# Kernel tuning notes

Hardware: AMD Instinct MI355X
Metric: run time of the kernel (lower is better)

Reference implementation:

```python
import jax, jax.numpy as jnp
import numpy as np
from jax import lax

C = 64
KD = 16  # in_channels // k_factor
KS = 3
DN = ('NCHW', 'OIHW', 'NCHW')


def setup_inputs() -> dict:
    key = jax.random.key(0)
    ks = jax.random.split(key, 9)
    B, H, W = 4, 128, 128
    s = 0.05
    return {
        'x': jax.random.normal(ks[0], (B, C, H, W), jnp.float32),
        'y': jax.random.normal(ks[1], (B, C, H, W), jnp.float32),
        'z': jax.random.normal(ks[2], (B, C, H, W), jnp.float32),
        'Wq': jax.random.normal(ks[3], (C, 1, KS, KS), jnp.float32) * s,   # depthwise
        'bq': jax.random.normal(ks[4], (C,), jnp.float32) * s,
        'Wk': jax.random.normal(ks[5], (KD, C, KS, KS), jnp.float32) * s,
        'bk': jax.random.normal(ks[6], (KD,), jnp.float32) * s,
        'wv': jax.random.normal(ks[7], (KD,), jnp.float32) * s,           # 1x1 conv 1->KD
        'bv': jax.random.normal(ks[8], (KD,), jnp.float32) * s,
    }


def reference(x, y, z, Wq, bq, Wk, bk, wv, bv):
    # Q: depthwise 3x3 conv + ReLU on y -> [B,C,H,W]
    q = jax.nn.relu(
        lax.conv_general_dilated(y, Wq, (1, 1), 'SAME',
                                 dimension_numbers=DN, feature_group_count=C)
        + bq[None, :, None, None])
    # K: 3x3 conv C->KD + ReLU on x -> [B,KD,H,W], shared across the C channel axis
    k = jax.nn.relu(
        lax.conv_general_dilated(x, Wk, (1, 1), 'SAME', dimension_numbers=DN)
        + bk[None, :, None, None])
    # V: 1x1 conv 1->KD + ReLU applied per input channel of z -> [B,C,KD,H,W]
    v = jax.nn.relu(z[:, :, None] * wv[None, None, :, None, None]
                    + bv[None, None, :, None, None])
    # Degenerate SDPA: head_dim=1 so scale=1; softmax over the KD 'sequence' axis.
    scores = q[:, :, None] * k[:, None]              # [B,C,KD,H,W]
    attn = jax.nn.softmax(scores, axis=2)
    return jnp.sum(attn * v, axis=2)                 # [B,C,H,W]
```

## Files before the change

### kernel.cpp

```cpp
#include <hip/hip_runtime.h>

#define HH 128
#define WW 128
#define CC 64
#define KD 16
#define HW (HH * WW)
#define HWB (HW * 4)
#define TOTBYTES (4u * CC * HW * 4u)
#define OOB_SENT 0x40000000

typedef __attribute__((ext_vector_type(4))) int   int32x4_t;
typedef __attribute__((ext_vector_type(4))) float floatx4;
typedef __attribute__((ext_vector_type(2))) float floatx2;

__device__ floatx4 llvm_amdgcn_raw_buffer_load_v4f32(int32x4_t srsrc, int voffset,
                                                     int soffset, int aux)
    __asm("llvm.amdgcn.raw.buffer.load.v4f32");
__device__ float llvm_amdgcn_raw_buffer_load_f32(int32x4_t srsrc, int voffset,
                                                 int soffset, int aux)
    __asm("llvm.amdgcn.raw.buffer.load.f32");

__device__ inline int32x4_t make_srd(const void* p, unsigned bytes) {
    const unsigned long long a = (unsigned long long)p;
    int32x4_t r;
    r.x = (int)(a & 0xffffffffull);
    r.y = (int)(a >> 32);
    r.z = (int)bytes;
    r.w = 0x00020000;
    return r;
}

#if __has_builtin(__builtin_amdgcn_exp2f)
#define FAST_EXP2(x) __builtin_amdgcn_exp2f(x)
#define KLOG2E 1.44269504088896340736f
#else
#define FAST_EXP2(x) __expf(x)
#define KLOG2E 1.0f
#endif

__global__ __launch_bounds__(512, 8) void gatev_fused(
    const float* __restrict__ x, const float* __restrict__ y,
    const float* __restrict__ z,
    const float* __restrict__ Wq, const float* __restrict__ bq,
    const float* __restrict__ Wk, const float* __restrict__ bk,
    const float* __restrict__ wv, const float* __restrict__ bv,
    float* __restrict__ out)
{
    __shared__ float wk_lds[9216];

    const int tid  = threadIdx.x;
    const int g    = __builtin_amdgcn_readfirstlane(tid >> 6);
    const int lane = tid & 63;
    const int px   = lane & 15, py = lane >> 4;
    const int b    = blockIdx.z;
    const int h    = blockIdx.y * 4 + py;
    const int w    = blockIdx.x * 16 + px;
    const int pix  = h * WW + w;

    const bool interior = (blockIdx.x > 0) & (blockIdx.x < 7) &
                          (blockIdx.y > 0) & (blockIdx.y < 31);

    const int32x4_t rx = make_srd(x, TOTBYTES);
    const int32x4_t ry = make_srd(y, TOTBYTES);
    const int32x4_t rz = make_srd(z, TOTBYTES);

    const int colb = (w > 0 ? w - 1 : 0) * 4;
    int rowB[3];
#pragma unroll
    for (int r = 0; r < 3; ++r) {
        const int rr = h - 1 + r;
        rowB[r] = (rr >= 0 && rr < HH) ? rr * WW * 4 + colb : OOB_SENT;
    }
    const float mL = (w > 0) ? 1.f : 0.f;
    const float mR = (w < WW - 1) ? 1.f : 0.f;
    const bool  w0e = (w == 0);

    const int base = b * CC * HWB;
    const int c0   = __builtin_amdgcn_readfirstlane(g * 8);

    {
        const int d  = tid & 15;
        const int cA = tid >> 4;
#pragma unroll
        for (int half = 0; half < 2; ++half) {
            const int c   = cA + half * 32;
            const int dst = (c >> 3) * 1152 + (c & 7) * 144 + d;
            const float* src = Wk + (d * CC + c) * 9;
#pragma unroll
            for (int t = 0; t < 9; ++t)
                wk_lds[dst + t * 16] = src[t];
        }
    }
    __syncthreads();

    floatx2 acc2[8];
#pragma unroll
    for (int p = 0; p < 8; ++p) acc2[p] = (floatx2){0.f, 0.f};

    auto load3 = [&](floatx4 (&f)[3], int so) {
#pragma unroll
        for (int r = 0; r < 3; ++r)
            f[r] = llvm_amdgcn_raw_buffer_load_v4f32(rx, rowB[r], so, 0);
    };
    auto taps3 = [&](const floatx4& f, float& tL, float& tC, float& tR) {
        if (interior) { tL = f.x; tC = f.y; tR = f.z; }
        else {
            tL = f.x * mL;
            tC = w0e ? f.x : f.y;
            tR = (w0e ? f.y : f.z) * mR;
        }
    };
    auto compute = [&](const floatx4 (&f)[3], int wb) {
        float tp[9];
#pragma unroll
        for (int r = 0; r < 3; ++r)
            taps3(f[r], tp[r * 3 + 0], tp[r * 3 + 1], tp[r * 3 + 2]);
#pragma unroll
        for (int t = 0; t < 9; ++t) {
            const floatx2 tp2 = {tp[t], tp[t]};
#pragma unroll
            for (int j = 0; j < 4; ++j) {
                const floatx4 w4 = *(const floatx4*)&wk_lds[wb + t * 16 + j * 4];
                const floatx2 lo = __builtin_shufflevector(w4, w4, 0, 1);
                const floatx2 hi = __builtin_shufflevector(w4, w4, 2, 3);
                acc2[2 * j + 0] = __builtin_elementwise_fma(lo, tp2, acc2[2 * j + 0]);
                acc2[2 * j + 1] = __builtin_elementwise_fma(hi, tp2, acc2[2 * j + 1]);
            }
        }
    };

    const int wbase = g * 1152;
    floatx4 f0[3], f1[3];
    load3(f0, base + c0 * HWB);
#pragma unroll
    for (int cp = 0; cp < 4; ++cp) {
        load3(f1, base + (c0 + 2 * cp + 1) * HWB);
        compute(f0, wbase + (2 * cp) * 144);
        load3(f0, base + (c0 + 2 * cp + 2) * HWB);
        compute(f1, wbase + (2 * cp + 1) * 144);
    }
    __syncthreads();

#pragma unroll
    for (int p = 0; p < 8; ++p) {
        wk_lds[g * 1024 + (2 * p + 0) * 64 + lane] = acc2[p].x;
        wk_lds[g * 1024 + (2 * p + 1) * 64 + lane] = acc2[p].y;
    }
    __syncthreads();

#pragma unroll
    for (int rep = 0; rep < 2; ++rep) {
        const int idx = tid + rep * 512;
        float s = wk_lds[idx];
#pragma unroll
        for (int gg = 1; gg < 8; ++gg) s += wk_lds[gg * 1024 + idx];
        const int d = idx >> 6;
        wk_lds[idx] = fmaxf(s + bk[d], 0.f) * KLOG2E;
    }
    __syncthreads();

    floatx2 qp[4], zp[4];
#pragma unroll 2
    for (int ci = 0; ci < 8; ++ci) {
        const int c  = c0 + ci;
        const int so = base + c * HWB;
        const float* wq = Wq + c * 9;
        float a = 0.f;
#pragma unroll
        for (int r = 0; r < 3; ++r) {
            const floatx4 f = llvm_amdgcn_raw_buffer_load_v4f32(ry, rowB[r], so, 0);
            float tL, tC, tR;
            taps3(f, tL, tC, tR);
            a = fmaf(wq[r * 3 + 0], tL, a);
            a = fmaf(wq[r * 3 + 1], tC, a);
            a = fmaf(wq[r * 3 + 2], tR, a);
        }
        qp[ci >> 1][ci & 1] = fmaxf(a + bq[c], 0.f);
        zp[ci >> 1][ci & 1] = llvm_amdgcn_raw_buffer_load_f32(rz, pix * 4, so, 0);
    }

    floatx2 num2[4], den2[4];
    const floatx2 zero2 = {0.f, 0.f};
#pragma unroll
    for (int p = 0; p < 4; ++p) { num2[p] = zero2; den2[p] = zero2; }

#pragma unroll
    for (int d = 0; d < KD; ++d) {
        const float kl  = wk_lds[d * 64 + lane];
        const floatx2 kl2 = {kl, kl};
        const float wvd = wv[d], bvd = bv[d];
        const floatx2 wv2 = {wvd, wvd}, bv2 = {bvd, bvd};
#pragma unroll
        for (int p = 0; p < 4; ++p) {
            const floatx2 s2 = qp[p] * kl2;
            floatx2 e2;
            e2.x = FAST_EXP2(s2.x);
            e2.y = FAST_EXP2(s2.y);
            const floatx2 v2 = __builtin_elementwise_max(
                __builtin_elementwise_fma(zp[p], wv2, bv2), zero2);
            num2[p] = __builtin_elementwise_fma(e2, v2, num2[p]);
            den2[p] = den2[p] + e2;
        }
    }

    float* ob = out + (size_t)b * CC * HW;
#pragma unroll
    for (int ci = 0; ci < 8; ++ci)
        ob[(c0 + ci) * HW + pix] =
            __fdividef(num2[ci >> 1][ci & 1], den2[ci >> 1][ci & 1]);
}

extern "C" void kernel_launch(void* const* d_in, const int* in_sizes, int n_in,
                              void* d_out, int out_size, void* d_ws, size_t ws_size,
                              hipStream_t stream) {
    const float* x  = (const float*)d_in[0];
    const float* y  = (const float*)d_in[1];
    const float* z  = (const float*)d_in[2];
    const float* Wq = (const float*)d_in[3];
    const float* bq = (const float*)d_in[4];
    const float* Wk = (const float*)d_in[5];
    const float* bk = (const float*)d_in[6];
    const float* wv = (const float*)d_in[7];
    const float* bv = (const float*)d_in[8];
    float* out = (float*)d_out;

    dim3 grid(WW / 16, HH / 4, 4);
    dim3 block(512);
    hipLaunchKernelGGL(gatev_fused, grid, block, 0, stream,
                       x, y, z, Wq, bq, Wk, bk, wv, bv, out);
}
```

Measured before the change: 50.49 us.

## Compute two adjacent pixels per thread to reuse conv taps and weights

Each thread now handles two horizontally adjacent pixels. A single float4 row load supplies the taps for both, and each LDS weight read feeds twice as many FMAs in the K conv. The Q/softmax phase is restructured into a per-channel double-buffered pipeline over y and z loads, with vectorized z loads and float2 output stores. The grid is halved, LDS grows to 64KB and launch bounds drop to 4 waves per EU, which raises register pressure and lowers occupancy.

```diff
diff --git a/kernel.cpp b/kernel.cpp
--- a/kernel.cpp
+++ b/kernel.cpp
@@ -16,9 +16,9 @@
 __device__ floatx4 llvm_amdgcn_raw_buffer_load_v4f32(int32x4_t srsrc, int voffset,
                                                      int soffset, int aux)
     __asm("llvm.amdgcn.raw.buffer.load.v4f32");
-__device__ float llvm_amdgcn_raw_buffer_load_f32(int32x4_t srsrc, int voffset,
-                                                 int soffset, int aux)
-    __asm("llvm.amdgcn.raw.buffer.load.f32");
+__device__ floatx2 llvm_amdgcn_raw_buffer_load_v2f32(int32x4_t srsrc, int voffset,
+                                                     int soffset, int aux)
+    __asm("llvm.amdgcn.raw.buffer.load.v2f32");
 
 __device__ inline int32x4_t make_srd(const void* p, unsigned bytes) {
     const unsigned long long a = (unsigned long long)p;
@@ -38,7 +38,7 @@
 #define KLOG2E 1.0f
 #endif
 
-__global__ __launch_bounds__(512, 8) void gatev_fused(
+__global__ __launch_bounds__(512, 4) void gatev_fused(
     const float* __restrict__ x, const float* __restrict__ y,
     const float* __restrict__ z,
     const float* __restrict__ Wq, const float* __restrict__ bq,
@@ -46,34 +46,32 @@
     const float* __restrict__ wv, const float* __restrict__ bv,
     float* __restrict__ out)
 {
-    __shared__ float wk_lds[9216];
+    __shared__ float lds[16384];
 
     const int tid  = threadIdx.x;
     const int g    = __builtin_amdgcn_readfirstlane(tid >> 6);
     const int lane = tid & 63;
-    const int px   = lane & 15, py = lane >> 4;
+    const int px16 = lane & 15, py = lane >> 4;
     const int b    = blockIdx.z;
+    const int w0   = blockIdx.x * 32 + px16 * 2;
     const int h    = blockIdx.y * 4 + py;
-    const int w    = blockIdx.x * 16 + px;
-    const int pix  = h * WW + w;
-
-    const bool interior = (blockIdx.x > 0) & (blockIdx.x < 7) &
-                          (blockIdx.y > 0) & (blockIdx.y < 31);
+    const int pix  = h * WW + w0;
+    const int p0   = py * 32 + px16 * 2;
 
     const int32x4_t rx = make_srd(x, TOTBYTES);
     const int32x4_t ry = make_srd(y, TOTBYTES);
     const int32x4_t rz = make_srd(z, TOTBYTES);
 
-    const int colb = (w > 0 ? w - 1 : 0) * 4;
+    const int colb = (w0 > 0 ? w0 - 1 : 0) * 4;
     int rowB[3];
 #pragma unroll
     for (int r = 0; r < 3; ++r) {
         const int rr = h - 1 + r;
         rowB[r] = (rr >= 0 && rr < HH) ? rr * WW * 4 + colb : OOB_SENT;
     }
-    const float mL = (w > 0) ? 1.f : 0.f;
-    const float mR = (w < WW - 1) ? 1.f : 0.f;
-    const bool  w0e = (w == 0);
+    const float mL = (w0 > 0) ? 1.f : 0.f;
+    const float mR = (w0 + 2 < WW) ? 1.f : 0.f;
+    const bool  w0e = (w0 == 0);
 
     const int base = b * CC * HWB;
     const int c0   = __builtin_amdgcn_readfirstlane(g * 8);
@@ -88,43 +86,44 @@
             const float* src = Wk + (d * CC + c) * 9;
 #pragma unroll
             for (int t = 0; t < 9; ++t)
-                wk_lds[dst + t * 16] = src[t];
-        }
-    }
-    __syncthreads();
-
-    floatx2 acc2[8];
-#pragma unroll
-    for (int p = 0; p < 8; ++p) acc2[p] = (floatx2){0.f, 0.f};
+                lds[dst + t * 16] = src[t];
+        }
+    }
+    __syncthreads();
+
+    floatx2 aP0[8], aP1[8];
+#pragma unroll
+    for (int i = 0; i < 8; ++i) { aP0[i] = (floatx2){0.f, 0.f}; aP1[i] = (floatx2){0.f, 0.f}; }
 
     auto load3 = [&](floatx4 (&f)[3], int so) {
 #pragma unroll
         for (int r = 0; r < 3; ++r)
             f[r] = llvm_amdgcn_raw_buffer_load_v4f32(rx, rowB[r], so, 0);
     };
-    auto taps3 = [&](const floatx4& f, float& tL, float& tC, float& tR) {
-        if (interior) { tL = f.x; tC = f.y; tR = f.z; }
-        else {
-            tL = f.x * mL;
-            tC = w0e ? f.x : f.y;
-            tR = (w0e ? f.y : f.z) * mR;
-        }
+    auto mktaps = [&](const floatx4& f, float (&s)[4]) {
+        s[0] = f.x * mL;
+        s[1] = w0e ? f.x : f.y;
+        s[2] = w0e ? f.y : f.z;
+        s[3] = (w0e ? f.z : f.w) * mR;
     };
     auto compute = [&](const floatx4 (&f)[3], int wb) {
-        float tp[9];
-#pragma unroll
-        for (int r = 0; r < 3; ++r)
-            taps3(f[r], tp[r * 3 + 0], tp[r * 3 + 1], tp[r * 3 + 2]);
+        float s[3][4];
+#pragma unroll
+        for (int r = 0; r < 3; ++r) mktaps(f[r], s[r]);
 #pragma unroll
         for (int t = 0; t < 9; ++t) {
-            const floatx2 tp2 = {tp[t], tp[t]};
+            const int tr = t / 3, tc = t % 3;
+            const floatx2 t0 = {s[tr][tc],     s[tr][tc]};
+            const floatx2 t1 = {s[tr][tc + 1], s[tr][tc + 1]};
 #pragma unroll
             for (int j = 0; j < 4; ++j) {
-                const floatx4 w4 = *(const floatx4*)&wk_lds[wb + t * 16 + j * 4];
+                const floatx4 w4 = *(const floatx4*)&lds[wb + t * 16 + j * 4];
                 const floatx2 lo = __builtin_shufflevector(w4, w4, 0, 1);
                 const floatx2 hi = __builtin_shufflevector(w4, w4, 2, 3);
-                acc2[2 * j + 0] = __builtin_elementwise_fma(lo, tp2, acc2[2 * j + 0]);
-                acc2[2 * j + 1] = __builtin_elementwise_fma(hi, tp2, acc2[2 * j + 1]);
+                aP0[2 * j + 0] = __builtin_elementwise_fma(lo, t0, aP0[2 * j + 0]);
+                aP0[2 * j + 1] = __builtin_elementwise_fma(hi, t0, aP0[2 * j + 1]);
+                aP1[2 * j + 0] = __builtin_elementwise_fma(lo, t1, aP1[2 * j + 0]);
+                aP1[2 * j + 1] = __builtin_elementwise_fma(hi, t1, aP1[2 * j + 1]);
             }
         }
     };
@@ -142,72 +141,81 @@
     __syncthreads();
 
 #pragma unroll
-    for (int p = 0; p < 8; ++p) {
-        wk_lds[g * 1024 + (2 * p + 0) * 64 + lane] = acc2[p].x;
-        wk_lds[g * 1024 + (2 * p + 1) * 64 + lane] = acc2[p].y;
-    }
-    __syncthreads();
-
-#pragma unroll
-    for (int rep = 0; rep < 2; ++rep) {
+    for (int i = 0; i < 8; ++i) {
+        *(floatx2*)&lds[g * 2048 + (2 * i + 0) * 128 + p0] = (floatx2){aP0[i].x, aP1[i].x};
+        *(floatx2*)&lds[g * 2048 + (2 * i + 1) * 128 + p0] = (floatx2){aP0[i].y, aP1[i].y};
+    }
+    __syncthreads();
+
+#pragma unroll
+    for (int rep = 0; rep < 4; ++rep) {
         const int idx = tid + rep * 512;
-        float s = wk_lds[idx];
-#pragma unroll
-        for (int gg = 1; gg < 8; ++gg) s += wk_lds[gg * 1024 + idx];
-        const int d = idx >> 6;
-        wk_lds[idx] = fmaxf(s + bk[d], 0.f) * KLOG2E;
-    }
-    __syncthreads();
-
-    floatx2 qp[4], zp[4];
-#pragma unroll 2
-    for (int ci = 0; ci < 8; ++ci) {
-        const int c  = c0 + ci;
-        const int so = base + c * HWB;
+        float s = lds[idx];
+#pragma unroll
+        for (int gg = 1; gg < 8; ++gg) s += lds[gg * 2048 + idx];
+        const int d = idx >> 7;
+        lds[idx] = fmaxf(s + bk[d], 0.f) * KLOG2E;
+    }
+    __syncthreads();
+
+    floatx2 kl2[16];
+#pragma unroll
+    for (int d = 0; d < KD; ++d)
+        kl2[d] = *(const floatx2*)&lds[d * 128 + p0];
+
+    auto process = [&](const floatx4 (&f)[3], floatx2 z2, int c) {
         const float* wq = Wq + c * 9;
-        float a = 0.f;
-#pragma unroll
-        for (int r = 0; r < 3; ++r) {
-            const floatx4 f = llvm_amdgcn_raw_buffer_load_v4f32(ry, rowB[r], so, 0);
-            float tL, tC, tR;
-            taps3(f, tL, tC, tR);
-            a = fmaf(wq[r * 3 + 0], tL, a);
-            a = fmaf(wq[r * 3 + 1], tC, a);
-            a = fmaf(wq[r * 3 + 2], tR, a);
-        }
-        qp[ci >> 1][ci & 1] = fmaxf(a + bq[c], 0.f);
-        zp[ci >> 1][ci & 1] = llvm_amdgcn_raw_buffer_load_f32(rz, pix * 4, so, 0);
-    }
-
-    floatx2 num2[4], den2[4];
-    const floatx2 zero2 = {0.f, 0.f};
-#pragma unroll
-    for (int p = 0; p < 4; ++p) { num2[p] = zero2; den2[p] = zero2; }
-
-#pragma unroll
-    for (int d = 0; d < KD; ++d) {
-        const float kl  = wk_lds[d * 64 + lane];
-        const floatx2 kl2 = {kl, kl};
-        const float wvd = wv[d], bvd = bv[d];
-        const floatx2 wv2 = {wvd, wvd}, bv2 = {bvd, bvd};
-#pragma unroll
-        for (int p = 0; p < 4; ++p) {
-            const floatx2 s2 = qp[p] * kl2;
+        float s[3][4];
+#pragma unroll
+        for (int r = 0; r < 3; ++r) mktaps(f[r], s[r]);
+        floatx2 q2 = {bq[c], bq[c]};
+#pragma unroll
+        for (int t = 0; t < 9; ++t) {
+            const int tr = t / 3, tc = t % 3;
+            const floatx2 tp2 = {s[tr][tc], s[tr][tc + 1]};
+            const floatx2 wq2 = {wq[t], wq[t]};
+            q2 = __builtin_elementwise_fma(wq2, tp2, q2);
+        }
+        const floatx2 zero2 = {0.f, 0.f};
+        q2 = __builtin_elementwise_max(q2, zero2);
+
+        floatx2 num2 = zero2, den2 = zero2;
+#pragma unroll
+        for (int d = 0; d < KD; ++d) {
+            const floatx2 s2 = q2 * kl2[d];
             floatx2 e2;
             e2.x = FAST_EXP2(s2.x);
             e2.y = FAST_EXP2(s2.y);
+            const floatx2 wv2 = {wv[d], wv[d]};
+            const floatx2 bv2 = {bv[d], bv[d]};
             const floatx2 v2 = __builtin_elementwise_max(
-                __builtin_elementwise_fma(zp[p], wv2, bv2), zero2);
-            num2[p] = __builtin_elementwise_fma(e2, v2, num2[p]);
-            den2[p] = den2[p] + e2;
-        }
-    }
-
-    float* ob = out + (size_t)b * CC * HW;
-#pragma unroll
-    for (int ci = 0; ci < 8; ++ci)
-        ob[(c0 + ci) * HW + pix] =
-            __fdividef(num2[ci >> 1][ci & 1], den2[ci >> 1][ci & 1]);
+                __builtin_elementwise_fma(z2, wv2, bv2), zero2);
+            num2 = __builtin_elementwise_fma(e2, v2, num2);
+            den2 = den2 + e2;
+        }
+        floatx2 o2;
+        o2.x = __fdividef(num2.x, den2.x);
+        o2.y = __fdividef(num2.y, den2.y);
+        *(floatx2*)&out[(size_t)b * CC * HW + (size_t)c * HW + pix] = o2;
+    };
+
+    floatx4 fy0[3], fy1[3];
+    floatx2 z0, z1;
+    auto load3y = [&](floatx4 (&f)[3], floatx2& zz, int so) {
+#pragma unroll
+        for (int r = 0; r < 3; ++r)
+            f[r] = llvm_amdgcn_raw_buffer_load_v4f32(ry, rowB[r], so, 0);
+        zz = llvm_amdgcn_raw_buffer_load_v2f32(rz, pix * 4, so, 0);
+    };
+
+    load3y(fy0, z0, base + c0 * HWB);
+#pragma unroll
+    for (int cp = 0; cp < 4; ++cp) {
+        load3y(fy1, z1, base + (c0 + 2 * cp + 1) * HWB);
+        process(fy0, z0, c0 + 2 * cp);
+        load3y(fy0, z0, base + (c0 + 2 * cp + 2) * HWB);
+        process(fy1, z1, c0 + 2 * cp + 1);
+    }
 }
 
 extern "C" void kernel_launch(void* const* d_in, const int* in_sizes, int n_in,
@@ -224,7 +232,7 @@
     const float* bv = (const float*)d_in[8];
     float* out = (float*)d_out;
 
-    dim3 grid(WW / 16, HH / 4, 4);
+    dim3 grid(WW / 32, HH / 4, 4);
     dim3 block(512);
     hipLaunchKernelGGL(gatev_fused, grid, block, 0, stream,
                        x, y, z, Wq, bq, Wk, bk, wv, bv, out);
```

New measurement: 43.45 us, median of 2. -13.9%, faster.
